# Performance work log

Measured on AMD Instinct MI355X. Metric: run time of the kernel, lower is better.

The kernel has to match this reference:

```python
import jax, jax.numpy as jnp
import numpy as np

B, T, C, H = 4, 2048, 1024, 16
D = C // H  # head_dim = 64


def setup_inputs() -> dict:
    key = jax.random.key(0)
    k1, k2, k3, k4 = jax.random.split(key, 4)
    x = jax.random.normal(k1, (B, T, C), dtype=jnp.float32)
    # realistic padding: each sequence has length in [T//2, T]
    lengths = jax.random.randint(k4, (B,), T // 2, T + 1)
    padding_mask = jnp.arange(T)[None, :] < lengths[:, None]  # True = keep
    # weights stored [in, out] (equivalent to torch Linear weight transposed)
    w_qkv = jax.random.normal(k2, (C, 3 * C), dtype=jnp.float32) * (C ** -0.5)
    w_out = jax.random.normal(k3, (C, C), dtype=jnp.float32) * (C ** -0.5)
    b_out = jnp.zeros((C,), dtype=jnp.float32)
    return {"x": x, "padding_mask": padding_mask, "w_qkv": w_qkv, "w_out": w_out, "b_out": b_out}


def reference(x, padding_mask, w_qkv, w_out, b_out):
    scale = D ** -0.5
    qkv = x @ w_qkv  # [B,T,3C]
    q, k, v = jnp.split(qkv, 3, axis=-1)

    def split_heads(t):
        return t.reshape(B, T, H, D).transpose(0, 2, 1, 3)  # [B,H,T,D]

    q, k, v = split_heads(q), split_heads(k), split_heads(v)
    attn = jnp.einsum("bhqd,bhkd->bhqk", q, k) * scale  # [B,H,T,T]
    mask = padding_mask[:, None, None, :]  # [B,1,1,T]
    attn = jnp.where(mask, attn, jnp.finfo(attn.dtype).min)
    attn = jax.nn.softmax(attn, axis=-1)
    # dropout is identity in eval mode
    out = jnp.einsum("bhqk,bhkd->bhqd", attn, v)  # [B,H,T,D]
    out = out.transpose(0, 2, 1, 3).reshape(B, T, C)
    return out @ w_out + b_out
```

## Files before the change

### kernel.cpp

```cpp
#include <hip/hip_runtime.h>
#include <hip/hip_bf16.h>

#define Bb 4
#define Tt 2048
#define Cc 1024
#define Hh 16

typedef unsigned short u16;
typedef __attribute__((ext_vector_type(8))) __bf16 bf16x8;
typedef __attribute__((ext_vector_type(4))) float  f32x4;

__device__ __forceinline__ u16 f2bf_hw(float f) {
    __bf16 h = (__bf16)f;
    return *(u16*)&h;
}

__device__ __forceinline__ unsigned cvt_pk_bf16(float a, float b) {
    unsigned r;
    asm("v_cvt_pk_bf16_f32 %0, %1, %2" : "=v"(r) : "v"(a), "v"(b));
    return r;
}

__device__ __forceinline__ float fexp2(float x) {
#if __has_builtin(__builtin_amdgcn_exp2f)
    return __builtin_amdgcn_exp2f(x);
#else
    return __expf(x * 0.6931471805599453f);
#endif
}

__device__ __forceinline__ void gld_lds16(const void* g, void* l) {
    __builtin_amdgcn_global_load_lds(
        (__attribute__((address_space(1))) void*)(g),
        (__attribute__((address_space(3))) void*)(l),
        16, 0, 0);
}

__device__ __forceinline__ f32x4 mfma16(bf16x8 a, bf16x8 b, f32x4 c) {
    return __builtin_amdgcn_mfma_f32_16x16x32_bf16(a, b, c, 0, 0, 0);
}

__global__ void cast_f32_bf16(const float* __restrict__ in, u16* __restrict__ out, int n4) {
    int i = blockIdx.x * 256 + threadIdx.x;
    if (i < n4) {
        float4 v = ((const float4*)in)[i];
        uint2 o;
        o.x = cvt_pk_bf16(v.x, v.y);
        o.y = cvt_pk_bf16(v.z, v.w);
        ((uint2*)out)[i] = o;
    }
}

__global__ void castT_f32_bf16(const float* __restrict__ in, u16* __restrict__ out,
                               int K, int N, int scaleN, float sv) {
    __shared__ float Ls[64][65];
    const int n0 = blockIdx.x * 64, k0 = blockIdx.y * 64;
    const int t = threadIdx.x;
    #pragma unroll
    for (int s = 0; s < 4; ++s) {
        int idx = t + 256 * s;
        int r   = idx >> 4;
        int c4  = (idx & 15) * 4;
        float4 v = *(const float4*)&in[(size_t)(k0 + r) * N + n0 + c4];
        Ls[r][c4 + 0] = v.x; Ls[r][c4 + 1] = v.y;
        Ls[r][c4 + 2] = v.z; Ls[r][c4 + 3] = v.w;
    }
    __syncthreads();
    #pragma unroll
    for (int s = 0; s < 2; ++s) {
        int idx = t + 256 * s;
        int n   = idx >> 3;
        int kc  = (idx & 7) * 8;
        const float sc = (n0 + n < scaleN) ? sv : 1.0f;
        alignas(16) u16 tmp[8];
        #pragma unroll
        for (int i = 0; i < 8; ++i) tmp[i] = f2bf_hw(Ls[kc + i][n] * sc);
        *(uint4*)&out[(size_t)(n0 + n) * K + k0 + kc] = *(const uint4*)tmp;
    }
}

__global__ void repack_frags(const u16* __restrict__ qkv,
                             u16* __restrict__ kx, u16* __restrict__ vx) {
    __shared__ u16 Kt[64 * 80];
    __shared__ u16 Vt[64 * 80];
    const int t = threadIdx.x;
    const int ch = blockIdx.x, bh = blockIdx.y, b = bh >> 4, h = bh & 15;
    const int kc = ch * 64;

    #pragma unroll
    for (int u = 0; u < 2; ++u) {
        int id = t + 256 * u;
        int key = id >> 3, c8 = id & 7;
        const size_t row = (size_t)(b * Tt + kc + key) * (3 * Cc) + h * 64 + c8 * 8;
        *(uint4*)&Kt[key * 80 + c8 * 8] = *(const uint4*)&qkv[row + Cc];
        *(uint4*)&Vt[key * 80 + c8 * 8] = *(const uint4*)&qkv[row + 2 * Cc];
    }
    __syncthreads();

    const size_t obase = (size_t)(bh * 32 + ch) * 4096;
    #pragma unroll
    for (int u = 0; u < 2; ++u) {
        int id = t + 256 * u;
        int lane = id & 63, ks = (id >> 6) & 1, jt = id >> 7;
        int l16 = lane & 15, quad = lane >> 4;
        uint4 kv = *(const uint4*)&Kt[(16 * jt + l16) * 80 + 32 * ks + quad * 8];
        *(uint4*)&kx[obase + (size_t)(jt * 2 + ks) * 512 + lane * 8] = kv;
        alignas(16) u16 tmp[8];
        #pragma unroll
        for (int j = 0; j < 8; ++j)
            tmp[j] = Vt[(32 * ks + quad * 8 + j) * 80 + 16 * jt + l16];
        *(uint4*)&vx[obase + (size_t)(jt * 2 + ks) * 512 + lane * 8] = *(const uint4*)tmp;
    }
}

__global__ __launch_bounds__(256, 3) void gemm_bt_bf16(
    const u16* __restrict__ A, const u16* __restrict__ Bt,
    const float* __restrict__ bias,
    u16* __restrict__ outB, float* __restrict__ outF,
    int M, int N, int K)
{
    __shared__ u16 As[128 * 32];
    __shared__ u16 Bs[128 * 32];
    const int t = threadIdx.x;
    const int w = t >> 6, lane = t & 63;
    const int quad = lane >> 4, l16 = lane & 15;
    const int wr = w >> 1, wc = w & 1;
    const int m0 = blockIdx.y * 128, n0 = blockIdx.x * 128;

    int aoff[4], boff[4];
    #pragma unroll
    for (int i = 0; i < 4; ++i) {
        int rA = 64 * wr + 16 * i + l16;
        aoff[i] = rA * 32 + ((quad ^ ((rA >> 1) & 3)) * 8);
        int rB = 64 * wc + 16 * i + l16;
        boff[i] = rB * 32 + ((quad ^ ((rB >> 1) & 3)) * 8);
    }

    f32x4 acc[4][4] = {};

    for (int k0 = 0; k0 < K; k0 += 32) {
        __syncthreads();
        #pragma unroll
        for (int u = 0; u < 2; ++u) {
            const int i   = 2 * w + u;
            const int row = 16 * i + (lane >> 2);
            const int c   = (lane & 3) ^ ((row >> 1) & 3);
            gld_lds16(A  + (size_t)(m0 + row) * K + k0 + c * 8, (void*)(As + i * 512 + lane * 8));
            gld_lds16(Bt + (size_t)(n0 + row) * K + k0 + c * 8, (void*)(Bs + i * 512 + lane * 8));
        }
        asm volatile("s_waitcnt vmcnt(0)" ::: "memory");
        __syncthreads();

        bf16x8 af[4], bfr[4];
        #pragma unroll
        for (int i = 0; i < 4; ++i) af[i]  = *(const bf16x8*)&As[aoff[i]];
        #pragma unroll
        for (int j = 0; j < 4; ++j) bfr[j] = *(const bf16x8*)&Bs[boff[j]];
        #pragma unroll
        for (int i = 0; i < 4; ++i)
            #pragma unroll
            for (int j = 0; j < 4; ++j)
                acc[i][j] = mfma16(af[i], bfr[j], acc[i][j]);
    }

    const int rbase = m0 + 64 * wr + quad * 4;
    const int cbase = n0 + 64 * wc + l16;
    if (outF) {
        float bv[4];
        #pragma unroll
        for (int j = 0; j < 4; ++j) bv[j] = bias[cbase + 16 * j];
        #pragma unroll
        for (int i = 0; i < 4; ++i)
            #pragma unroll
            for (int r = 0; r < 4; ++r) {
                size_t ro = (size_t)(rbase + 16 * i + r) * N;
                #pragma unroll
                for (int j = 0; j < 4; ++j)
                    outF[ro + cbase + 16 * j] = acc[i][j][r] + bv[j];
            }
    } else {
        #pragma unroll
        for (int i = 0; i < 4; ++i)
            #pragma unroll
            for (int r = 0; r < 4; ++r) {
                size_t ro = (size_t)(rbase + 16 * i + r) * N;
                #pragma unroll
                for (int j = 0; j < 4; ++j)
                    outB[ro + cbase + 16 * j] = f2bf_hw(acc[i][j][r]);
            }
    }
}

#define PH_PRE()  do { __builtin_amdgcn_s_barrier();                        \
                       asm volatile("s_waitcnt lgkmcnt(0)" ::: "memory");   \
                       __builtin_amdgcn_sched_barrier(0);                   \
                       __builtin_amdgcn_s_setprio(1); } while (0)
#define PH_POST() do { __builtin_amdgcn_s_setprio(0);                       \
                       __builtin_amdgcn_s_barrier(); } while (0)

__global__ __launch_bounds__(512, 2) void gemm_bt_256(
    const u16* __restrict__ A, const u16* __restrict__ Bt,
    u16* __restrict__ out, int M, int N, int K)
{
    __shared__ u16 sm[65536];
    const int t = threadIdx.x;
    const int w = t >> 6, lane = t & 63;
    const int quad = lane >> 4, l16 = lane & 15;
    const int wm = w >> 2, wn = w & 3;

    const int gx   = gridDim.x;
    const int nwg  = gx * gridDim.y;
    const int orig = blockIdx.y * gx + blockIdx.x;
    const int wg   = (orig & 7) * (nwg >> 3) + (orig >> 3);
    const int bn = wg % gx, bm = wg / gx;
    const int m0 = bm << 8, n0 = bn << 8;
    const int NKT = K >> 6;

    const int l8r   = lane >> 3;
    const int g_log = (lane & 7) ^ l8r;
    const u16* sAp[4]; const u16* sBp[4];
    #pragma unroll
    for (int u = 0; u < 4; ++u) {
        const int gi = w * 4 + u;
        sAp[u] = A  + (size_t)(m0 + gi * 8 + l8r) * K + g_log * 8;
        sBp[u] = Bt + (size_t)(n0 + gi * 8 + l8r) * K + g_log * 8;
    }
    const int dst0 = w * 2048 + lane * 8;

    auto STAGE = [&](int tt, int u, int p) {
        const int tc = (tt < NKT) ? tt : (NKT - 1);
        const size_t ko = (size_t)tc << 6;
        u16* d = sm + p * 32768 + dst0 + u * 512;
        gld_lds16(sAp[u] + ko, d);
        gld_lds16(sBp[u] + ko, d + 16384);
    };

    const int x7   = l16 & 7;
    const int rowA = (wm * 128 + l16) * 64;
    const int rowB = (wn * 64  + l16) * 64;
    const int sw0  = (quad ^ x7) * 8;
    const int sw1  = ((4 + quad) ^ x7) * 8;
    const int a00 = rowA + sw0, a01 = rowA + sw1;
    const int b00 = rowB + sw0, b01 = rowB + sw1;

    f32x4 acc[8][4] = {};

    STAGE(0, 0, 0); STAGE(0, 1, 0); STAGE(0, 2, 0); STAGE(0, 3, 0);
    STAGE(1, 0, 1);
    asm volatile("s_waitcnt vmcnt(2)" ::: "memory");
    __builtin_amdgcn_s_barrier();

    for (int kt = 0; kt < NKT; ++kt) {
        const int p = kt & 1;
        const u16* LA = sm + p * 32768;
        const u16* LB = LA + 16384;
        bf16x8 ar0[4], ar1[4], br0[4], br1[4];

        #pragma unroll
        for (int m = 0; m < 4; ++m) ar0[m] = *(const bf16x8*)&LA[a00 + m * 1024];
        #pragma unroll
        for (int n = 0; n < 4; ++n) br0[n] = *(const bf16x8*)&LB[b00 + n * 1024];
        STAGE(kt + 1, 1, p ^ 1);
        PH_PRE();
        #pragma unroll
        for (int m = 0; m < 4; ++m)
            #pragma unroll
            for (int n = 0; n < 4; ++n)
                acc[m][n] = mfma16(ar0[m], br0[n], acc[m][n]);
        PH_POST();

        #pragma unroll
        for (int m = 0; m < 4; ++m) ar1[m] = *(const bf16x8*)&LA[a00 + (4 + m) * 1024];
        #pragma unroll
        for (int n = 0; n < 4; ++n) br1[n] = *(const bf16x8*)&LB[b01 + n * 1024];
        STAGE(kt + 1, 2, p ^ 1);
        PH_PRE();
        #pragma unroll
        for (int m = 0; m < 4; ++m)
            #pragma unroll
            for (int n = 0; n < 4; ++n)
                acc[4 + m][n] = mfma16(ar1[m], br0[n], acc[4 + m][n]);
        PH_POST();

        #pragma unroll
        for (int m = 0; m < 4; ++m) ar0[m] = *(const bf16x8*)&LA[a01 + m * 1024];
        #pragma unroll
        for (int m = 0; m < 4; ++m) ar1[m] = *(const bf16x8*)&LA[a01 + (4 + m) * 1024];
        STAGE(kt + 1, 3, p ^ 1);
        PH_PRE();
        #pragma unroll
        for (int m = 0; m < 4; ++m)
            #pragma unroll
            for (int n = 0; n < 4; ++n)
                acc[m][n] = mfma16(ar0[m], br1[n], acc[m][n]);
        PH_POST();

        STAGE(kt + 2, 0, p);
        PH_PRE();
        #pragma unroll
        for (int m = 0; m < 4; ++m)
            #pragma unroll
            for (int n = 0; n < 4; ++n)
                acc[4 + m][n] = mfma16(ar1[m], br1[n], acc[4 + m][n]);
        __builtin_amdgcn_s_setprio(0);
        asm volatile("s_waitcnt vmcnt(2)" ::: "memory");
        __builtin_amdgcn_s_barrier();
    }

    const int rb = m0 + wm * 128 + quad * 4;
    const int cb = n0 + wn * 64 + l16;
    #pragma unroll
    for (int m = 0; m < 8; ++m)
        #pragma unroll
        for (int r = 0; r < 4; ++r) {
            const size_t ro = (size_t)(rb + m * 16 + r) * N;
            #pragma unroll
            for (int n = 0; n < 4; ++n)
                out[ro + cb + n * 16] = f2bf_hw(acc[m][n][r]);
        }
}

__global__ __launch_bounds__(64, 2) void attn_mfma(
    const u16* __restrict__ qkv, const u16* __restrict__ kx, const u16* __restrict__ vx,
    const int* __restrict__ mask, u16* __restrict__ outO)
{
    __shared__ u16 Ps[64 * 68];

    const int lane = threadIdx.x;
    const int quad = lane >> 4, l16 = lane & 15;
    const int bh = blockIdx.x, qt = blockIdx.y, b = bh >> 4, h = bh & 15;

    int sum = 0;
    {
        const int4* mp = (const int4*)(mask + b * Tt) + lane * 8;
        #pragma unroll
        for (int i = 0; i < 8; ++i) { int4 m4 = mp[i]; sum += m4.x + m4.y + m4.z + m4.w; }
        #pragma unroll
        for (int off = 1; off < 64; off <<= 1) sum += __shfl_xor(sum, off);
    }
    const int L = sum;

    const int q0 = qt * 64;
    bf16x8 qf[4][2];
    #pragma unroll
    for (int qq = 0; qq < 4; ++qq) {
        const u16* qp = qkv + (size_t)(b * Tt + q0 + 16 * qq + l16) * (3 * Cc) + h * 64 + quad * 8;
        qf[qq][0] = *(const bf16x8*)(qp);
        qf[qq][1] = *(const bf16x8*)(qp + 32);
    }

    f32x4 oacc[4][4] = {};
    f32x4 lacc[4]    = {};
    const __bf16 onebf = (__bf16)1.0f;
    const bf16x8 ones  = {onebf, onebf, onebf, onebf, onebf, onebf, onebf, onebf};

    const int nfull = L >> 6;
    const int nch   = (L + 63) >> 6;
    const size_t fb = (size_t)bh * 32 * 4096 + lane * 8;

    uint4 kf[4][2];
    #pragma unroll
    for (int jt = 0; jt < 4; ++jt)
        #pragma unroll
        for (int ks = 0; ks < 2; ++ks)
            kf[jt][ks] = *(const uint4*)&kx[fb + (size_t)(jt * 2 + ks) * 512];

    for (int ch = 0; ch < nch; ++ch) {
        uint4 vf[4][2];
        #pragma unroll
        for (int jt = 0; jt < 4; ++jt)
            #pragma unroll
            for (int ks = 0; ks < 2; ++ks)
                vf[jt][ks] = *(const uint4*)&vx[fb + (size_t)ch * 4096 + (size_t)(jt * 2 + ks) * 512];

        #pragma unroll
        for (int qq = 0; qq < 4; ++qq) {
            f32x4 st[4];
            #pragma unroll
            for (int jt = 0; jt < 4; ++jt) {
                f32x4 z = {0.f, 0.f, 0.f, 0.f};
                z = mfma16(*(const bf16x8*)&kf[jt][0], qf[qq][0], z);
                st[jt] = mfma16(*(const bf16x8*)&kf[jt][1], qf[qq][1], z);
            }
            uint2 pk[4];
            if (ch < nfull) {
                #pragma unroll
                for (int jt = 0; jt < 4; ++jt) {
                    pk[jt].x = cvt_pk_bf16(fexp2(st[jt][0]), fexp2(st[jt][1]));
                    pk[jt].y = cvt_pk_bf16(fexp2(st[jt][2]), fexp2(st[jt][3]));
                }
            } else {
                const int kc = ch * 64;
                #pragma unroll
                for (int jt = 0; jt < 4; ++jt) {
                    const int kb = kc + 16 * jt + quad * 4;
                    float e[4];
                    #pragma unroll
                    for (int r = 0; r < 4; ++r)
                        e[r] = (kb + r < L) ? fexp2(st[jt][r]) : 0.f;
                    pk[jt].x = cvt_pk_bf16(e[0], e[1]);
                    pk[jt].y = cvt_pk_bf16(e[2], e[3]);
                }
            }
            #pragma unroll
            for (int jt = 0; jt < 4; ++jt)
                *(uint2*)&Ps[(16 * qq + l16) * 68 + 16 * jt + quad * 4] = pk[jt];
        }

        {
            const int chn = (ch + 1 < nch) ? ch + 1 : ch;
            #pragma unroll
            for (int jt = 0; jt < 4; ++jt)
                #pragma unroll
                for (int ks = 0; ks < 2; ++ks)
                    kf[jt][ks] = *(const uint4*)&kx[fb + (size_t)chn * 4096 + (size_t)(jt * 2 + ks) * 512];
        }

        #pragma unroll
        for (int qq = 0; qq < 4; ++qq) {
            #pragma unroll
            for (int ks = 0; ks < 2; ++ks) {
                const u16* pr = &Ps[(16 * qq + l16) * 68 + 32 * ks + quad * 8];
                uint2 pa = *(const uint2*)pr;
                uint2 pb = *(const uint2*)(pr + 4);
                uint4 comb = {pa.x, pa.y, pb.x, pb.y};
                bf16x8 pf = *(const bf16x8*)&comb;
                #pragma unroll
                for (int dt = 0; dt < 4; ++dt)
                    oacc[qq][dt] = mfma16(pf, *(const bf16x8*)&vf[dt][ks], oacc[qq][dt]);
                lacc[qq] = mfma16(pf, ones, lacc[qq]);
            }
        }
    }

    #pragma unroll
    for (int qq = 0; qq < 4; ++qq)
        #pragma unroll
        for (int r = 0; r < 4; ++r) {
            const float inv = 1.f / lacc[qq][r];
            const size_t ro = (size_t)(b * Tt + q0 + 16 * qq + quad * 4 + r) * Cc + h * 64 + l16;
            #pragma unroll
            for (int dt = 0; dt < 4; ++dt)
                outO[ro + 16 * dt] = f2bf_hw(oacc[qq][dt][r] * inv);
        }
}

extern "C" void kernel_launch(void* const* d_in, const int* in_sizes, int n_in,
                              void* d_out, int out_size, void* d_ws, size_t ws_size,
                              hipStream_t stream) {
    const float* x     = (const float*)d_in[0];
    const int*   mask  = (const int*)  d_in[1];
    const float* w_qkv = (const float*)d_in[2];
    const float* w_out = (const float*)d_in[3];
    const float* b_out = (const float*)d_in[4];
    float*       outp  = (float*)d_out;

    const int M = Bb * Tt;
    char* ws = (char*)d_ws;
    u16* xb     = (u16*)(ws);
    u16* wqkvT  = (u16*)(ws + (16u << 20));
    u16* woutT  = (u16*)(ws + (22u << 20));
    u16* qkv    = (u16*)(ws + (24u << 20));
    u16* kx     = (u16*)(ws + (72u << 20));
    u16* vx     = (u16*)(ws + (88u << 20));
    u16* attnO  = (u16*)(ws);

    const float c2 = 0.18033688011112042f;

    cast_f32_bf16<<<(M * Cc / 4 + 255) / 256, 256, 0, stream>>>(x, xb, M * Cc / 4);
    castT_f32_bf16<<<dim3(3 * Cc / 64, Cc / 64), 256, 0, stream>>>(w_qkv, wqkvT, Cc, 3 * Cc, Cc, c2);
    castT_f32_bf16<<<dim3(Cc / 64, Cc / 64), 256, 0, stream>>>(w_out, woutT, Cc, Cc, 0, 1.0f);

    gemm_bt_256<<<dim3(3 * Cc / 256, M / 256), 512, 0, stream>>>(
        xb, wqkvT, qkv, M, 3 * Cc, Cc);

    repack_frags<<<dim3(Tt / 64, Bb * Hh), 256, 0, stream>>>(qkv, kx, vx);

    attn_mfma<<<dim3(Bb * Hh, Tt / 64), 64, 0, stream>>>(qkv, kx, vx, mask, attnO);

    gemm_bt_bf16<<<dim3(Cc / 128, M / 128), 256, 0, stream>>>(
        attnO, woutT, b_out, nullptr, outp, M, Cc, Cc);
}
```

Before: 263.4 us.

## Share K/V chunks across four waves via LDS double buffer; batch GEMM stage loads

The attention kernel moves from one 64-thread wave per 64-query tile to 256-thread blocks of four waves covering 256 queries. The waves share K/V chunks loaded into a double-buffered LDS area with direct global-to-LDS loads, so global K/V traffic per query drops to a quarter. This adds a block barrier per chunk and more LDS use, and leaves a grid of only 512 blocks. The QKV GEMM now issues all four prefetch stages for tile kt+2 at once at the end of each iteration, instead of spreading them across the MFMA phases, and waits with vmcnt(8).

```diff
diff --git a/kernel.cpp b/kernel.cpp
--- a/kernel.cpp
+++ b/kernel.cpp
@@ -246,8 +246,8 @@
     f32x4 acc[8][4] = {};
 
     STAGE(0, 0, 0); STAGE(0, 1, 0); STAGE(0, 2, 0); STAGE(0, 3, 0);
-    STAGE(1, 0, 1);
-    asm volatile("s_waitcnt vmcnt(2)" ::: "memory");
+    STAGE(1, 0, 1); STAGE(1, 1, 1); STAGE(1, 2, 1); STAGE(1, 3, 1);
+    asm volatile("s_waitcnt vmcnt(8)" ::: "memory");
     __builtin_amdgcn_s_barrier();
 
     for (int kt = 0; kt < NKT; ++kt) {
@@ -260,7 +260,6 @@
         for (int m = 0; m < 4; ++m) ar0[m] = *(const bf16x8*)&LA[a00 + m * 1024];
         #pragma unroll
         for (int n = 0; n < 4; ++n) br0[n] = *(const bf16x8*)&LB[b00 + n * 1024];
-        STAGE(kt + 1, 1, p ^ 1);
         PH_PRE();
         #pragma unroll
         for (int m = 0; m < 4; ++m)
@@ -273,7 +272,6 @@
         for (int m = 0; m < 4; ++m) ar1[m] = *(const bf16x8*)&LA[a00 + (4 + m) * 1024];
         #pragma unroll
         for (int n = 0; n < 4; ++n) br1[n] = *(const bf16x8*)&LB[b01 + n * 1024];
-        STAGE(kt + 1, 2, p ^ 1);
         PH_PRE();
         #pragma unroll
         for (int m = 0; m < 4; ++m)
@@ -286,7 +284,6 @@
         for (int m = 0; m < 4; ++m) ar0[m] = *(const bf16x8*)&LA[a01 + m * 1024];
         #pragma unroll
         for (int m = 0; m < 4; ++m) ar1[m] = *(const bf16x8*)&LA[a01 + (4 + m) * 1024];
-        STAGE(kt + 1, 3, p ^ 1);
         PH_PRE();
         #pragma unroll
         for (int m = 0; m < 4; ++m)
@@ -295,7 +292,8 @@
                 acc[m][n] = mfma16(ar0[m], br1[n], acc[m][n]);
         PH_POST();
 
-        STAGE(kt + 2, 0, p);
+        STAGE(kt + 2, 0, p); STAGE(kt + 2, 1, p);
+        STAGE(kt + 2, 2, p); STAGE(kt + 2, 3, p);
         PH_PRE();
         #pragma unroll
         for (int m = 0; m < 4; ++m)
@@ -303,9 +301,10 @@
             for (int n = 0; n < 4; ++n)
                 acc[4 + m][n] = mfma16(ar1[m], br1[n], acc[4 + m][n]);
         __builtin_amdgcn_s_setprio(0);
-        asm volatile("s_waitcnt vmcnt(2)" ::: "memory");
+        asm volatile("s_waitcnt vmcnt(8)" ::: "memory");
         __builtin_amdgcn_s_barrier();
     }
+    asm volatile("s_waitcnt vmcnt(0)" ::: "memory");
 
     const int rb = m0 + wm * 128 + quad * 4;
     const int cb = n0 + wn * 64 + l16;
@@ -320,15 +319,17 @@
         }
 }
 
-__global__ __launch_bounds__(64, 2) void attn_mfma(
+__global__ __launch_bounds__(256, 2) void attn_mfma4(
     const u16* __restrict__ qkv, const u16* __restrict__ kx, const u16* __restrict__ vx,
     const int* __restrict__ mask, u16* __restrict__ outO)
 {
-    __shared__ u16 Ps[64 * 68];
-
-    const int lane = threadIdx.x;
+    __shared__ u16 KVs[2][8192];
+    __shared__ u16 Pss[4][64 * 68];
+
+    const int t = threadIdx.x;
+    const int w = t >> 6, lane = t & 63;
     const int quad = lane >> 4, l16 = lane & 15;
-    const int bh = blockIdx.x, qt = blockIdx.y, b = bh >> 4, h = bh & 15;
+    const int bh = blockIdx.x, qb = blockIdx.y, b = bh >> 4, h = bh & 15;
 
     int sum = 0;
     {
@@ -340,7 +341,7 @@
     }
     const int L = sum;
 
-    const int q0 = qt * 64;
+    const int q0 = qb * 256 + w * 64;
     bf16x8 qf[4][2];
     #pragma unroll
     for (int qq = 0; qq < 4; ++qq) {
@@ -356,22 +357,42 @@
 
     const int nfull = L >> 6;
     const int nch   = (L + 63) >> 6;
-    const size_t fb = (size_t)bh * 32 * 4096 + lane * 8;
-
-    uint4 kf[4][2];
-    #pragma unroll
-    for (int jt = 0; jt < 4; ++jt)
-        #pragma unroll
-        for (int ks = 0; ks < 2; ++ks)
-            kf[jt][ks] = *(const uint4*)&kx[fb + (size_t)(jt * 2 + ks) * 512];
+    const size_t cb0 = (size_t)bh * 32 * 4096;
+    u16* Pw = Pss[w];
+
+    {
+        const u16* ksrc = kx + cb0;
+        const u16* vsrc = vx + cb0;
+        gld_lds16(ksrc + t * 8,        &KVs[0][t * 8]);
+        gld_lds16(ksrc + 2048 + t * 8, &KVs[0][2048 + t * 8]);
+        gld_lds16(vsrc + t * 8,        &KVs[0][4096 + t * 8]);
+        gld_lds16(vsrc + 2048 + t * 8, &KVs[0][6144 + t * 8]);
+    }
+    __syncthreads();
 
     for (int ch = 0; ch < nch; ++ch) {
-        uint4 vf[4][2];
+        const int p = ch & 1;
+
+        {
+            const int cc = (ch + 1 < nch) ? ch + 1 : ch;
+            const u16* ksrc = kx + cb0 + (size_t)cc * 4096;
+            const u16* vsrc = vx + cb0 + (size_t)cc * 4096;
+            u16* d = KVs[p ^ 1];
+            gld_lds16(ksrc + t * 8,        d + t * 8);
+            gld_lds16(ksrc + 2048 + t * 8, d + 2048 + t * 8);
+            gld_lds16(vsrc + t * 8,        d + 4096 + t * 8);
+            gld_lds16(vsrc + 2048 + t * 8, d + 6144 + t * 8);
+        }
+
+        const u16* Kb = KVs[p];
+        const u16* Vb = KVs[p] + 4096;
+
+        bf16x8 kf[4][2];
         #pragma unroll
         for (int jt = 0; jt < 4; ++jt)
             #pragma unroll
             for (int ks = 0; ks < 2; ++ks)
-                vf[jt][ks] = *(const uint4*)&vx[fb + (size_t)ch * 4096 + (size_t)(jt * 2 + ks) * 512];
+                kf[jt][ks] = *(const bf16x8*)&Kb[(jt * 2 + ks) * 512 + lane * 8];
 
         #pragma unroll
         for (int qq = 0; qq < 4; ++qq) {
@@ -379,8 +400,8 @@
             #pragma unroll
             for (int jt = 0; jt < 4; ++jt) {
                 f32x4 z = {0.f, 0.f, 0.f, 0.f};
-                z = mfma16(*(const bf16x8*)&kf[jt][0], qf[qq][0], z);
-                st[jt] = mfma16(*(const bf16x8*)&kf[jt][1], qf[qq][1], z);
+                z = mfma16(kf[jt][0], qf[qq][0], z);
+                st[jt] = mfma16(kf[jt][1], qf[qq][1], z);
             }
             uint2 pk[4];
             if (ch < nfull) {
@@ -404,33 +425,33 @@
             }
             #pragma unroll
             for (int jt = 0; jt < 4; ++jt)
-                *(uint2*)&Ps[(16 * qq + l16) * 68 + 16 * jt + quad * 4] = pk[jt];
+                *(uint2*)&Pw[(16 * qq + l16) * 68 + 16 * jt + quad * 4] = pk[jt];
         }
 
-        {
-            const int chn = (ch + 1 < nch) ? ch + 1 : ch;
-            #pragma unroll
-            for (int jt = 0; jt < 4; ++jt)
-                #pragma unroll
-                for (int ks = 0; ks < 2; ++ks)
-                    kf[jt][ks] = *(const uint4*)&kx[fb + (size_t)chn * 4096 + (size_t)(jt * 2 + ks) * 512];
-        }
+        bf16x8 vf[4][2];
+        #pragma unroll
+        for (int dt = 0; dt < 4; ++dt)
+            #pragma unroll
+            for (int ks = 0; ks < 2; ++ks)
+                vf[dt][ks] = *(const bf16x8*)&Vb[(dt * 2 + ks) * 512 + lane * 8];
 
         #pragma unroll
         for (int qq = 0; qq < 4; ++qq) {
             #pragma unroll
             for (int ks = 0; ks < 2; ++ks) {
-                const u16* pr = &Ps[(16 * qq + l16) * 68 + 32 * ks + quad * 8];
+                const u16* pr = &Pw[(16 * qq + l16) * 68 + 32 * ks + quad * 8];
                 uint2 pa = *(const uint2*)pr;
                 uint2 pb = *(const uint2*)(pr + 4);
                 uint4 comb = {pa.x, pa.y, pb.x, pb.y};
                 bf16x8 pf = *(const bf16x8*)&comb;
                 #pragma unroll
                 for (int dt = 0; dt < 4; ++dt)
-                    oacc[qq][dt] = mfma16(pf, *(const bf16x8*)&vf[dt][ks], oacc[qq][dt]);
+                    oacc[qq][dt] = mfma16(pf, vf[dt][ks], oacc[qq][dt]);
                 lacc[qq] = mfma16(pf, ones, lacc[qq]);
             }
         }
+
+        __syncthreads();
     }
 
     #pragma unroll
@@ -476,7 +497,7 @@
 
     repack_frags<<<dim3(Tt / 64, Bb * Hh), 256, 0, stream>>>(qkv, kx, vx);
 
-    attn_mfma<<<dim3(Bb * Hh, Tt / 64), 64, 0, stream>>>(qkv, kx, vx, mask, attnO);
+    attn_mfma4<<<dim3(Bb * Hh, Tt / 256), 256, 0, stream>>>(qkv, kx, vx, mask, attnO);
 
     gemm_bt_bf16<<<dim3(Cc / 128, M / 128), 256, 0, stream>>>(
         attnO, woutT, b_out, nullptr, outp, M, Cc, Cc);
```

After: 275.8 us. 4.7% more time.
